# Optimization experiments

Hardware: AMD Instinct MI355X
Metric: run time of the kernel (lower is better)

The kernel has to match this reference:

```python
import jax, jax.numpy as jnp
import numpy as np

D_MODEL = 2048
NUM_HEADS = 32
NUM_KV_HEADS = 8
HEAD_DIM = D_MODEL // NUM_HEADS
ROPE_BASE = 10000.0


def _rope_cos_sin(T, dtype):
    # standard LLaMA-style RoPE tables, shape (1, 1, T, head_dim)
    half = HEAD_DIM // 2
    inv_freq = 1.0 / (ROPE_BASE ** (jnp.arange(0, half, dtype=jnp.float32) / half))
    pos = jnp.arange(T, dtype=jnp.float32)
    freqs = pos[:, None] * inv_freq[None, :]          # (T, half)
    emb = jnp.concatenate([freqs, freqs], axis=-1)     # (T, head_dim)
    cos = jnp.cos(emb)[None, None].astype(dtype)
    sin = jnp.sin(emb)[None, None].astype(dtype)
    return cos, sin


def _rotate_half(x):
    h = x.shape[-1] // 2
    return jnp.concatenate([-x[..., h:], x[..., :h]], axis=-1)


def setup_inputs() -> dict:
    key = jax.random.key(0)
    ks = jax.random.split(key, 5)
    B, T = 2, 2048
    s = 1.0 / np.sqrt(D_MODEL)
    return {
        "x": jax.random.normal(ks[0], (B, T, D_MODEL), jnp.float32),
        "Wq": jax.random.normal(ks[1], (D_MODEL, D_MODEL), jnp.float32) * s,
        "Wk": jax.random.normal(ks[2], (NUM_KV_HEADS * HEAD_DIM, D_MODEL), jnp.float32) * s,
        "Wv": jax.random.normal(ks[3], (NUM_KV_HEADS * HEAD_DIM, D_MODEL), jnp.float32) * s,
        "Wo": jax.random.normal(ks[4], (D_MODEL, D_MODEL), jnp.float32) * s,
    }


def reference(x, Wq, Wk, Wv, Wo):
    B, T, _ = x.shape
    # projections (torch Linear: y = x @ W.T)
    Q = (x @ Wq.T).reshape(B, T, NUM_HEADS, HEAD_DIM).transpose(0, 2, 1, 3)      # (B,H,T,D)
    K = (x @ Wk.T).reshape(B, T, NUM_KV_HEADS, HEAD_DIM).transpose(0, 2, 1, 3)   # (B,Hkv,T,D)
    V = (x @ Wv.T).reshape(B, T, NUM_KV_HEADS, HEAD_DIM).transpose(0, 2, 1, 3)

    cos, sin = _rope_cos_sin(T, x.dtype)
    Q = Q * cos + _rotate_half(Q) * sin
    K = K * cos + _rotate_half(K) * sin

    # GQA: expand kv heads to query heads
    heads_per_kv = NUM_HEADS // NUM_KV_HEADS
    group_map = jnp.arange(NUM_HEADS) // heads_per_kv
    K_sel = K[:, group_map]  # (B,H,T,D)
    V_sel = V[:, group_map]

    scale = 1.0 / np.sqrt(HEAD_DIM)
    scores = jnp.einsum("bhqd,bhkd->bhqk", Q, K_sel) * scale
    causal = jnp.tril(jnp.ones((T, T), dtype=bool))
    scores = jnp.where(causal, scores, jnp.finfo(scores.dtype).min)
    attn = jax.nn.softmax(scores, axis=-1)
    out = jnp.einsum("bhqk,bhkd->bhqd", attn, V_sel)
    out = out.transpose(0, 2, 1, 3).reshape(B, T, D_MODEL)
    return out @ Wo.T
```

## Files before the change

kernel.cpp:

```cpp
#include <hip/hip_runtime.h>
#include <stdint.h>


typedef unsigned short u16;
typedef __attribute__((ext_vector_type(8))) short short8;
typedef __attribute__((ext_vector_type(4))) float floatx4;

#define T_SEQ 2048
#define DMODEL 2048
#define NHEADS 32
#define KVHEADS 8
#define HDIM 64

__device__ __forceinline__ u16 f2bf(float f) {
  uint32_t u = __builtin_bit_cast(uint32_t, f);
  u = (u + 0x7FFFu + ((u >> 16) & 1u)) >> 16;
  return (u16)u;
}
__device__ __forceinline__ float bf2f(u16 h) {
  uint32_t u = ((uint32_t)h) << 16;
  return __builtin_bit_cast(float, u);
}

__device__ __forceinline__ void gld_lds16(const void* g, void* l) {
  __builtin_amdgcn_global_load_lds(
      (const __attribute__((address_space(1))) unsigned int*)g,
      (__attribute__((address_space(3))) unsigned int*)l, 16, 0, 0);
}

__global__ __launch_bounds__(256) void cvt_kernel(const float* __restrict__ src,
                                                  u16* __restrict__ dst, int n4) {
  int i = blockIdx.x * 256 + threadIdx.x;
  if (i >= n4) return;
  float4 v = ((const float4*)src)[i];
  ushort4 o;
  o.x = f2bf(v.x); o.y = f2bf(v.y); o.z = f2bf(v.z); o.w = f2bf(v.w);
  ((ushort4*)dst)[i] = o;
}

__global__ __launch_bounds__(256) void rope_table_kernel(float* __restrict__ cosT,
                                                         float* __restrict__ sinT) {
  int idx = blockIdx.x * 256 + threadIdx.x;
  int t = idx >> 5, i = idx & 31;
  float invf = 1.0f / powf(10000.0f, (float)i / 32.0f);
  float a = (float)t * invf;
  cosT[idx] = cosf(a);
  sinT[idx] = sinf(a);
}

template <bool OUT_F32>
__global__ __launch_bounds__(256) void gemm_bt(const u16* __restrict__ A,
                                               const u16* __restrict__ Bm,
                                               float* __restrict__ Cf,
                                               u16* __restrict__ Cb,
                                               int M, int N, int K) {
  __shared__ u16 As[128 * 64];
  __shared__ u16 Bs[128 * 64];
  const int tid = threadIdx.x;
  const int lane = tid & 63;
  const int wid = tid >> 6;
  const int wr = wid >> 1, wc = wid & 1;
  const long bm = (long)blockIdx.y * 128;
  const long bn = (long)blockIdx.x * 128;

  floatx4 acc[4][4] = {};

  for (int kt = 0; kt < K; kt += 64) {
#pragma unroll
    for (int c = 0; c < 4; ++c) {
      int g = (wid * 4 + c) * 64 + lane;
      int row = g >> 3, slot = g & 7;
      int ss = slot ^ (row & 7);
      gld_lds16(A + (bm + row) * (long)K + kt + ss * 8, (char*)As + g * 16);
      gld_lds16(Bm + (bn + row) * (long)K + kt + ss * 8, (char*)Bs + g * 16);
    }
    __syncthreads();
#pragma unroll
    for (int ks = 0; ks < 2; ++ks) {
      short8 af[4], bfr[4];
#pragma unroll
      for (int m = 0; m < 4; ++m) {
        int row = wr * 64 + m * 16 + (lane & 15);
        int slot = (ks * 4 + (lane >> 4)) ^ (row & 7);
        af[m] = *(const short8*)((const char*)As + row * 128 + slot * 16);
      }
#pragma unroll
      for (int n = 0; n < 4; ++n) {
        int row = wc * 64 + n * 16 + (lane & 15);
        int slot = (ks * 4 + (lane >> 4)) ^ (row & 7);
        bfr[n] = *(const short8*)((const char*)Bs + row * 128 + slot * 16);
      }
#pragma unroll
      for (int m = 0; m < 4; ++m)
#pragma unroll
        for (int n = 0; n < 4; ++n)
          acc[m][n] = __builtin_amdgcn_mfma_f32_16x16x32_bf16(af[m], bfr[n],
                                                              acc[m][n], 0, 0, 0);
    }
    __syncthreads();
  }
#pragma unroll
  for (int m = 0; m < 4; ++m)
#pragma unroll
    for (int n = 0; n < 4; ++n)
#pragma unroll
      for (int r = 0; r < 4; ++r) {
        long row = bm + wr * 64 + m * 16 + (lane >> 4) * 4 + r;
        long col = bn + wc * 64 + n * 16 + (lane & 15);
        if constexpr (OUT_F32)
          Cf[row * N + col] = acc[m][n][r];
        else
          Cb[row * N + col] = f2bf(acc[m][n][r]);
      }
}

__global__ __launch_bounds__(256) void rope_apply_kernel(
    const u16* __restrict__ QKV, const float* __restrict__ cosT,
    const float* __restrict__ sinT, u16* __restrict__ Qh, u16* __restrict__ Kh) {
  int idx = blockIdx.x * 256 + threadIdx.x;
  int c = idx % 2560;
  int bt = idx / 2560;
  int t = bt & (T_SEQ - 1);
  int b = bt >> 11;
  int hd = c & 63;
  int i = hd & 31;
  float cs = cosT[t * 32 + i];
  float sn = sinT[t * 32 + i];
  long base = (long)bt * 3072;
  float xv = bf2f(QKV[base + c]);
  int pairc = (hd < 32) ? c + 32 : c - 32;
  float xp = bf2f(QKV[base + pairc]);
  float rot = (hd < 32) ? -xp : xp;
  float ov = xv * cs + rot * sn;
  if (c < 2048) {
    int h = c >> 6;
    Qh[((long)(b * NHEADS + h) * T_SEQ + t) * HDIM + hd] = f2bf(ov);
  } else {
    int kv = (c - 2048) >> 6;
    Kh[((long)(b * KVHEADS + kv) * T_SEQ + t) * HDIM + hd] = f2bf(ov);
  }
}

__global__ __launch_bounds__(256) void v_transpose_kernel(const u16* __restrict__ QKV,
                                                          u16* __restrict__ Vt) {
  __shared__ u16 tl[64 * 65];
  int blk = blockIdx.x;
  int ttile = blk & 31;
  int kvh = (blk >> 5) & 7;
  int b = blk >> 8;
  int tid = threadIdx.x;
  long bt0 = (long)b * T_SEQ + ttile * 64;
#pragma unroll
  for (int j = 0; j < 2; ++j) {
    int chunk = tid * 2 + j;
    int el = chunk * 8;
    int row = el >> 6, col = el & 63;
    short8 v = *(const short8*)(QKV + (bt0 + row) * 3072 + 2560 + kvh * 64 + col);
#pragma unroll
    for (int k = 0; k < 8; ++k) tl[(col + k) * 65 + row] = (u16)v[k];
  }
  __syncthreads();
#pragma unroll
  for (int j = 0; j < 2; ++j) {
    int chunk = tid * 2 + j;
    int el = chunk * 8;
    int d = el >> 6, t0 = el & 63;
    short8 o;
#pragma unroll
    for (int k = 0; k < 8; ++k) o[k] = (short)tl[d * 65 + t0 + k];
    *(short8*)(Vt + ((long)(b * KVHEADS + kvh) * HDIM + d) * T_SEQ + ttile * 64 + t0) = o;
  }
}

__global__ __launch_bounds__(256) void attn_kernel(const u16* __restrict__ Qh,
                                                   const u16* __restrict__ Kh,
                                                   const u16* __restrict__ Vt,
                                                   u16* __restrict__ O) {
  __shared__ u16 Ks[64 * 64];
  __shared__ u16 Vs[64 * 64];
  __shared__ u16 Ps[4 * 1024];
  const int tid = threadIdx.x;
  const int lane = tid & 63;
  const int w = tid >> 6;
  const int blk = blockIdx.x;
  const int qb = blk & 31;
  const int h = (blk >> 5) & 31;
  const int b = blk >> 10;
  const int kvh = h >> 2;
  const int qbase = qb * 64;
  const int l15 = lane & 15;
  const int l4 = lane >> 4;

  const u16* Qp = Qh + ((long)(b * NHEADS + h) * T_SEQ + qbase + w * 16 + l15) * HDIM;
  short8 qf0 = *(const short8*)(Qp + l4 * 8);
  short8 qf1 = *(const short8*)(Qp + 32 + l4 * 8);
  const u16* Kbase = Kh + (long)(b * KVHEADS + kvh) * T_SEQ * HDIM;
  const u16* Vbase = Vt + (long)(b * KVHEADS + kvh) * HDIM * T_SEQ;

  float m_run = -1e30f, l_run = 0.f;
  floatx4 oA[4] = {};
  const int qg = qbase + w * 16 + l15;
  char* Pw = (char*)Ps + w * 2048;

  for (int kt = 0; kt <= qb; ++kt) {
#pragma unroll
    for (int c = 0; c < 2; ++c) {
      int g = (w * 2 + c) * 64 + lane;
      int row = g >> 3, slot = g & 7;
      int ss = slot ^ (row & 7);
      gld_lds16(Kbase + (long)(kt * 64 + row) * HDIM + ss * 8, (char*)Ks + g * 16);
      gld_lds16(Vbase + (long)row * T_SEQ + kt * 64 + ss * 8, (char*)Vs + g * 16);
    }
    __syncthreads();

    floatx4 st[4] = {};
#pragma unroll
    for (int ks = 0; ks < 2; ++ks) {
      short8 qf = ks ? qf1 : qf0;
#pragma unroll
      for (int tt = 0; tt < 4; ++tt) {
        int row = tt * 16 + l15;
        int slot = (ks * 4 + l4) ^ (row & 7);
        short8 kf = *(const short8*)((const char*)Ks + row * 128 + slot * 16);
        st[tt] = __builtin_amdgcn_mfma_f32_16x16x32_bf16(kf, qf, st[tt], 0, 0, 0);
      }
    }

    float p[4][4];
    float mt = -1e30f;
#pragma unroll
    for (int tt = 0; tt < 4; ++tt)
#pragma unroll
      for (int r = 0; r < 4; ++r) {
        int tg = kt * 64 + tt * 16 + l4 * 4 + r;
        float v = st[tt][r] * 0.125f;
        v = (tg <= qg) ? v : -1e30f;
        p[tt][r] = v;
        mt = fmaxf(mt, v);
      }
    mt = fmaxf(mt, __shfl_xor(mt, 16));
    mt = fmaxf(mt, __shfl_xor(mt, 32));
    float m_new = fmaxf(m_run, mt);
    float alpha = __expf(m_run - m_new);
    float lsum = 0.f;
#pragma unroll
    for (int tt = 0; tt < 4; ++tt)
#pragma unroll
      for (int r = 0; r < 4; ++r) {
        float e = __expf(p[tt][r] - m_new);
        p[tt][r] = e;
        lsum += e;
      }
    lsum += __shfl_xor(lsum, 16);
    lsum += __shfl_xor(lsum, 32);
    l_run = l_run * alpha + lsum;
    m_run = m_new;

#pragma unroll
    for (int tt = 0; tt < 4; ++tt) {
      uint2 pk;
      pk.x = (uint32_t)f2bf(p[tt][0]) | ((uint32_t)f2bf(p[tt][1]) << 16);
      pk.y = (uint32_t)f2bf(p[tt][2]) | ((uint32_t)f2bf(p[tt][3]) << 16);
      int t0 = tt * 16 + l4 * 4;
      int slot = (t0 >> 3) ^ (l15 & 7);
      int half = (t0 & 4) ? 8 : 0;
      *(uint2*)(Pw + l15 * 128 + slot * 16 + half) = pk;
    }
    asm volatile("s_waitcnt lgkmcnt(0)" ::: "memory");

    float a0 = __shfl(alpha, l4 * 4 + 0);
    float a1 = __shfl(alpha, l4 * 4 + 1);
    float a2 = __shfl(alpha, l4 * 4 + 2);
    float a3 = __shfl(alpha, l4 * 4 + 3);
#pragma unroll
    for (int dd = 0; dd < 4; ++dd) {
      oA[dd][0] *= a0; oA[dd][1] *= a1; oA[dd][2] *= a2; oA[dd][3] *= a3;
    }
#pragma unroll
    for (int ks2 = 0; ks2 < 2; ++ks2) {
      int slotp = (ks2 * 4 + l4) ^ (l15 & 7);
      short8 pa = *(const short8*)(Pw + l15 * 128 + slotp * 16);
#pragma unroll
      for (int dd = 0; dd < 4; ++dd) {
        int row = dd * 16 + l15;
        int slot = (ks2 * 4 + l4) ^ (row & 7);
        short8 vb = *(const short8*)((const char*)Vs + row * 128 + slot * 16);
        oA[dd] = __builtin_amdgcn_mfma_f32_16x16x32_bf16(pa, vb, oA[dd], 0, 0, 0);
      }
    }
    __syncthreads();
  }

  float linv = 1.0f / l_run;
  float i0 = __shfl(linv, l4 * 4 + 0);
  float i1 = __shfl(linv, l4 * 4 + 1);
  float i2 = __shfl(linv, l4 * 4 + 2);
  float i3 = __shfl(linv, l4 * 4 + 3);
  float iv[4] = {i0, i1, i2, i3};
#pragma unroll
  for (int dd = 0; dd < 4; ++dd)
#pragma unroll
    for (int r = 0; r < 4; ++r) {
      int trow = qbase + w * 16 + l4 * 4 + r;
      int col = h * 64 + dd * 16 + l15;
      O[((long)b * T_SEQ + trow) * DMODEL + col] = f2bf(oA[dd][r] * iv[r]);
    }
}

extern "C" void kernel_launch(void* const* d_in, const int* in_sizes, int n_in,
                              void* d_out, int out_size, void* d_ws, size_t ws_size,
                              hipStream_t stream) {
  const float* x = (const float*)d_in[0];
  const float* Wq = (const float*)d_in[1];
  const float* Wk = (const float*)d_in[2];
  const float* Wv = (const float*)d_in[3];
  const float* Wo = (const float*)d_in[4];
  float* out = (float*)d_out;

  char* ws = (char*)d_ws;
  u16* x_bf = (u16*)(ws);
  u16* Obuf = (u16*)(ws);
  u16* Wqkv_bf = (u16*)(ws + 16777216);
  u16* Wo_bf = (u16*)(ws + 29360128);
  u16* QKV = (u16*)(ws + 37748736);
  u16* Qh = (u16*)(ws + 62914560);
  u16* Kh = (u16*)(ws + 79691776);
  u16* Vt = (u16*)(ws + 83886080);
  float* cosT = (float*)(ws + 88080384);
  float* sinT = (float*)(ws + 88342528);

  cvt_kernel<<<8192, 256, 0, stream>>>(x, x_bf, 2097152);
  cvt_kernel<<<4096, 256, 0, stream>>>(Wq, Wqkv_bf, 1048576);
  cvt_kernel<<<1024, 256, 0, stream>>>(Wk, Wqkv_bf + 2048 * 2048, 262144);
  cvt_kernel<<<1024, 256, 0, stream>>>(Wv, Wqkv_bf + 2560 * 2048, 262144);
  cvt_kernel<<<4096, 256, 0, stream>>>(Wo, Wo_bf, 1048576);
  rope_table_kernel<<<256, 256, 0, stream>>>(cosT, sinT);

  dim3 g1(24, 32);
  gemm_bt<false><<<g1, 256, 0, stream>>>(x_bf, Wqkv_bf, nullptr, QKV, 4096, 3072, 2048);

  rope_apply_kernel<<<40960, 256, 0, stream>>>(QKV, cosT, sinT, Qh, Kh);
  v_transpose_kernel<<<512, 256, 0, stream>>>(QKV, Vt);

  attn_kernel<<<2048, 256, 0, stream>>>(Qh, Kh, Vt, Obuf);

  dim3 g2(16, 32);
  gemm_bt<true><<<g2, 256, 0, stream>>>(Obuf, Wo_bf, out, nullptr, 4096, 2048, 2048);
}
```

Measured before the change: 392.5 us.

## Double-buffer K/V tiles, reverse block order, and defer softmax rescaling

The attention kernel now double-buffers K/V tiles in LDS, prefetching the next tile while computing the current one. A single barrier per iteration replaces the previous sync-after-load pattern. Blocks are issued heaviest-first (reversed q-block order) to balance the causal workload. The causal mask is applied only on the diagonal tile, and the online-softmax rescale is skipped when the running max grows by no more than a threshold. MFMA sections also get s_setprio. The extra buffers double K/V LDS use, which may reduce occupancy, and deferred rescaling relies on bounded exponent growth for accuracy.

```diff
diff --git a/kernel.cpp b/kernel.cpp
--- a/kernel.cpp
+++ b/kernel.cpp
@@ -176,14 +176,14 @@
                                                    const u16* __restrict__ Kh,
                                                    const u16* __restrict__ Vt,
                                                    u16* __restrict__ O) {
-  __shared__ u16 Ks[64 * 64];
-  __shared__ u16 Vs[64 * 64];
+  __shared__ u16 Ks[2][64 * 64];
+  __shared__ u16 Vs[2][64 * 64];
   __shared__ u16 Ps[4 * 1024];
   const int tid = threadIdx.x;
   const int lane = tid & 63;
   const int w = tid >> 6;
   const int blk = blockIdx.x;
-  const int qb = blk & 31;
+  const int qb = 31 - (blk & 31);
   const int h = (blk >> 5) & 31;
   const int b = blk >> 10;
   const int kvh = h >> 2;
@@ -202,18 +202,33 @@
   const int qg = qbase + w * 16 + l15;
   char* Pw = (char*)Ps + w * 2048;
 
-  for (int kt = 0; kt <= qb; ++kt) {
+  auto STAGE = [&](int kt, int buf) {
 #pragma unroll
     for (int c = 0; c < 2; ++c) {
       int g = (w * 2 + c) * 64 + lane;
       int row = g >> 3, slot = g & 7;
       int ss = slot ^ (row & 7);
-      gld_lds16(Kbase + (long)(kt * 64 + row) * HDIM + ss * 8, (char*)Ks + g * 16);
-      gld_lds16(Vbase + (long)row * T_SEQ + kt * 64 + ss * 8, (char*)Vs + g * 16);
-    }
-    __syncthreads();
+      gld_lds16(Kbase + (long)(kt * 64 + row) * HDIM + ss * 8,
+                (char*)Ks[buf] + g * 16);
+      gld_lds16(Vbase + (long)row * T_SEQ + kt * 64 + ss * 8,
+                (char*)Vs[buf] + g * 16);
+    }
+  };
+
+  STAGE(0, 0);
+  asm volatile("s_waitcnt vmcnt(0)" ::: "memory");
+  __builtin_amdgcn_s_barrier();
+  asm volatile("" ::: "memory");
+
+  for (int kt = 0; kt <= qb; ++kt) {
+    const int cur = kt & 1;
+    if (kt < qb) STAGE(kt + 1, cur ^ 1);
+
+    const char* Kc = (const char*)Ks[cur];
+    const char* Vc = (const char*)Vs[cur];
 
     floatx4 st[4] = {};
+    __builtin_amdgcn_s_setprio(1);
 #pragma unroll
     for (int ks = 0; ks < 2; ++ks) {
       short8 qf = ks ? qf1 : qf0;
@@ -221,40 +236,60 @@
       for (int tt = 0; tt < 4; ++tt) {
         int row = tt * 16 + l15;
         int slot = (ks * 4 + l4) ^ (row & 7);
-        short8 kf = *(const short8*)((const char*)Ks + row * 128 + slot * 16);
+        short8 kf = *(const short8*)(Kc + row * 128 + slot * 16);
         st[tt] = __builtin_amdgcn_mfma_f32_16x16x32_bf16(kf, qf, st[tt], 0, 0, 0);
       }
     }
+    __builtin_amdgcn_s_setprio(0);
 
     float p[4][4];
     float mt = -1e30f;
-#pragma unroll
-    for (int tt = 0; tt < 4; ++tt)
-#pragma unroll
-      for (int r = 0; r < 4; ++r) {
-        int tg = kt * 64 + tt * 16 + l4 * 4 + r;
-        float v = st[tt][r] * 0.125f;
-        v = (tg <= qg) ? v : -1e30f;
-        p[tt][r] = v;
-        mt = fmaxf(mt, v);
-      }
+    if (kt == qb) {
+#pragma unroll
+      for (int tt = 0; tt < 4; ++tt)
+#pragma unroll
+        for (int r = 0; r < 4; ++r) {
+          int tg = kt * 64 + tt * 16 + l4 * 4 + r;
+          float v = st[tt][r] * 0.125f;
+          v = (tg <= qg) ? v : -1e30f;
+          p[tt][r] = v;
+          mt = fmaxf(mt, v);
+        }
+    } else {
+#pragma unroll
+      for (int tt = 0; tt < 4; ++tt)
+#pragma unroll
+        for (int r = 0; r < 4; ++r) {
+          float v = st[tt][r] * 0.125f;
+          p[tt][r] = v;
+          mt = fmaxf(mt, v);
+        }
+    }
     mt = fmaxf(mt, __shfl_xor(mt, 16));
     mt = fmaxf(mt, __shfl_xor(mt, 32));
-    float m_new = fmaxf(m_run, mt);
-    float alpha = __expf(m_run - m_new);
+
+    bool defer = __all(mt - m_run <= 8.0f);
+    float m_use, alpha;
+    if (defer) {
+      m_use = m_run;
+      alpha = 1.0f;
+    } else {
+      m_use = fmaxf(m_run, mt);
+      alpha = __expf(m_run - m_use);
+    }
     float lsum = 0.f;
 #pragma unroll
     for (int tt = 0; tt < 4; ++tt)
 #pragma unroll
       for (int r = 0; r < 4; ++r) {
-        float e = __expf(p[tt][r] - m_new);
+        float e = __expf(p[tt][r] - m_use);
         p[tt][r] = e;
         lsum += e;
       }
     lsum += __shfl_xor(lsum, 16);
     lsum += __shfl_xor(lsum, 32);
     l_run = l_run * alpha + lsum;
-    m_run = m_new;
+    m_run = m_use;
 
 #pragma unroll
     for (int tt = 0; tt < 4; ++tt) {
@@ -268,14 +303,17 @@
     }
     asm volatile("s_waitcnt lgkmcnt(0)" ::: "memory");
 
-    float a0 = __shfl(alpha, l4 * 4 + 0);
-    float a1 = __shfl(alpha, l4 * 4 + 1);
-    float a2 = __shfl(alpha, l4 * 4 + 2);
-    float a3 = __shfl(alpha, l4 * 4 + 3);
-#pragma unroll
-    for (int dd = 0; dd < 4; ++dd) {
-      oA[dd][0] *= a0; oA[dd][1] *= a1; oA[dd][2] *= a2; oA[dd][3] *= a3;
-    }
+    if (!defer) {
+      float a0 = __shfl(alpha, l4 * 4 + 0);
+      float a1 = __shfl(alpha, l4 * 4 + 1);
+      float a2 = __shfl(alpha, l4 * 4 + 2);
+      float a3 = __shfl(alpha, l4 * 4 + 3);
+#pragma unroll
+      for (int dd = 0; dd < 4; ++dd) {
+        oA[dd][0] *= a0; oA[dd][1] *= a1; oA[dd][2] *= a2; oA[dd][3] *= a3;
+      }
+    }
+    __builtin_amdgcn_s_setprio(1);
 #pragma unroll
     for (int ks2 = 0; ks2 < 2; ++ks2) {
       int slotp = (ks2 * 4 + l4) ^ (l15 & 7);
@@ -284,11 +322,15 @@
       for (int dd = 0; dd < 4; ++dd) {
         int row = dd * 16 + l15;
         int slot = (ks2 * 4 + l4) ^ (row & 7);
-        short8 vb = *(const short8*)((const char*)Vs + row * 128 + slot * 16);
+        short8 vb = *(const short8*)(Vc + row * 128 + slot * 16);
         oA[dd] = __builtin_amdgcn_mfma_f32_16x16x32_bf16(pa, vb, oA[dd], 0, 0, 0);
       }
     }
-    __syncthreads();
+    __builtin_amdgcn_s_setprio(0);
+
+    asm volatile("s_waitcnt vmcnt(0)" ::: "memory");
+    __builtin_amdgcn_s_barrier();
+    asm volatile("" ::: "memory");
   }
 
   float linv = 1.0f / l_run;
```

Result: faster. 376.8 us (-4.0%).

## Restructure attention loop: direct global K/V loads, exp2 softmax, lazy rescale, swizzle

Applied to the files above, without the earlier changes.

Folds the softmax scale and log2(e) into Q during the RoPE step so the attention loop can use exp2 directly. The attention kernel drops the shared-memory K/V staging and the block-wide barriers, and each wave now reads K and V fragments straight from global memory through the cache. It adds a deferred-max rescale that skips the alpha multiply when the running max grows by at most 8, applies the causal mask only on the diagonal tile, and adds MFMA priority hints. Blocks are reordered so the longest query tiles run first and neighbouring blocks share KV heads. The trade-off is redundant global/L2 traffic across the four waves in place of one shared LDS copy, and looser numeric bounds on the unnormalised exponentials.

```diff
diff --git a/kernel.cpp b/kernel.cpp
--- a/kernel.cpp
+++ b/kernel.cpp
@@ -11,6 +11,7 @@
 #define NHEADS 32
 #define KVHEADS 8
 #define HDIM 64
+#define QK_SCALE 0.1803368801111204f
 
 __device__ __forceinline__ u16 f2bf(float f) {
   uint32_t u = __builtin_bit_cast(uint32_t, f);
@@ -134,7 +135,7 @@
   float ov = xv * cs + rot * sn;
   if (c < 2048) {
     int h = c >> 6;
-    Qh[((long)(b * NHEADS + h) * T_SEQ + t) * HDIM + hd] = f2bf(ov);
+    Qh[((long)(b * NHEADS + h) * T_SEQ + t) * HDIM + hd] = f2bf(ov * QK_SCALE);
   } else {
     int kv = (c - 2048) >> 6;
     Kh[((long)(b * KVHEADS + kv) * T_SEQ + t) * HDIM + hd] = f2bf(ov);
@@ -172,20 +173,19 @@
   }
 }
 
-__global__ __launch_bounds__(256) void attn_kernel(const u16* __restrict__ Qh,
-                                                   const u16* __restrict__ Kh,
-                                                   const u16* __restrict__ Vt,
-                                                   u16* __restrict__ O) {
-  __shared__ u16 Ks[64 * 64];
-  __shared__ u16 Vs[64 * 64];
+__global__ __launch_bounds__(256, 4) void attn_kernel(const u16* __restrict__ Qh,
+                                                      const u16* __restrict__ Kh,
+                                                      const u16* __restrict__ Vt,
+                                                      u16* __restrict__ O) {
   __shared__ u16 Ps[4 * 1024];
   const int tid = threadIdx.x;
   const int lane = tid & 63;
   const int w = tid >> 6;
-  const int blk = blockIdx.x;
-  const int qb = blk & 31;
-  const int h = (blk >> 5) & 31;
-  const int b = blk >> 10;
+  const int blk0 = blockIdx.x;
+  const int swz = (blk0 & 7) * 256 + (blk0 >> 3);
+  const int qb = 31 - (swz & 31);
+  const int h = (swz >> 5) & 31;
+  const int b = swz >> 10;
   const int kvh = h >> 2;
   const int qbase = qb * 64;
   const int l15 = lane & 15;
@@ -203,64 +203,64 @@
   char* Pw = (char*)Ps + w * 2048;
 
   for (int kt = 0; kt <= qb; ++kt) {
-#pragma unroll
-    for (int c = 0; c < 2; ++c) {
-      int g = (w * 2 + c) * 64 + lane;
-      int row = g >> 3, slot = g & 7;
-      int ss = slot ^ (row & 7);
-      gld_lds16(Kbase + (long)(kt * 64 + row) * HDIM + ss * 8, (char*)Ks + g * 16);
-      gld_lds16(Vbase + (long)row * T_SEQ + kt * 64 + ss * 8, (char*)Vs + g * 16);
-    }
-    __syncthreads();
+    const u16* Kt = Kbase + (long)kt * 64 * HDIM;
+    const u16* Vti = Vbase + kt * 64;
 
     floatx4 st[4] = {};
+    __builtin_amdgcn_s_setprio(1);
 #pragma unroll
     for (int ks = 0; ks < 2; ++ks) {
       short8 qf = ks ? qf1 : qf0;
 #pragma unroll
       for (int tt = 0; tt < 4; ++tt) {
-        int row = tt * 16 + l15;
-        int slot = (ks * 4 + l4) ^ (row & 7);
-        short8 kf = *(const short8*)((const char*)Ks + row * 128 + slot * 16);
+        short8 kf = *(const short8*)(Kt + (tt * 16 + l15) * HDIM + ks * 32 + l4 * 8);
         st[tt] = __builtin_amdgcn_mfma_f32_16x16x32_bf16(kf, qf, st[tt], 0, 0, 0);
       }
     }
-
-    float p[4][4];
-    float mt = -1e30f;
-#pragma unroll
-    for (int tt = 0; tt < 4; ++tt)
-#pragma unroll
-      for (int r = 0; r < 4; ++r) {
-        int tg = kt * 64 + tt * 16 + l4 * 4 + r;
-        float v = st[tt][r] * 0.125f;
-        v = (tg <= qg) ? v : -1e30f;
-        p[tt][r] = v;
-        mt = fmaxf(mt, v);
-      }
+    __builtin_amdgcn_s_setprio(0);
+
+    if (kt == qb) {
+#pragma unroll
+      for (int tt = 0; tt < 4; ++tt)
+#pragma unroll
+        for (int r = 0; r < 4; ++r) {
+          int tg = kt * 64 + tt * 16 + l4 * 4 + r;
+          if (tg > qg) st[tt][r] = -1e30f;
+        }
+    }
+    float mx0 = fmaxf(fmaxf(st[0][0], st[0][1]), fmaxf(st[0][2], st[0][3]));
+    float mx1 = fmaxf(fmaxf(st[1][0], st[1][1]), fmaxf(st[1][2], st[1][3]));
+    float mx2 = fmaxf(fmaxf(st[2][0], st[2][1]), fmaxf(st[2][2], st[2][3]));
+    float mx3 = fmaxf(fmaxf(st[3][0], st[3][1]), fmaxf(st[3][2], st[3][3]));
+    float mt = fmaxf(fmaxf(mx0, mx1), fmaxf(mx2, mx3));
     mt = fmaxf(mt, __shfl_xor(mt, 16));
     mt = fmaxf(mt, __shfl_xor(mt, 32));
-    float m_new = fmaxf(m_run, mt);
-    float alpha = __expf(m_run - m_new);
-    float lsum = 0.f;
-#pragma unroll
-    for (int tt = 0; tt < 4; ++tt)
-#pragma unroll
-      for (int r = 0; r < 4; ++r) {
-        float e = __expf(p[tt][r] - m_new);
-        p[tt][r] = e;
-        lsum += e;
-      }
+
+    bool defer = __all(mt - m_run <= 8.0f);
+    float m_use = defer ? m_run : fmaxf(m_run, mt);
+    float alpha = defer ? 1.0f : exp2f(m_run - m_use);
+
+    float lsp[4];
+#pragma unroll
+    for (int tt = 0; tt < 4; ++tt) {
+      float e0 = exp2f(st[tt][0] - m_use);
+      float e1 = exp2f(st[tt][1] - m_use);
+      float e2 = exp2f(st[tt][2] - m_use);
+      float e3 = exp2f(st[tt][3] - m_use);
+      st[tt][0] = e0; st[tt][1] = e1; st[tt][2] = e2; st[tt][3] = e3;
+      lsp[tt] = (e0 + e1) + (e2 + e3);
+    }
+    float lsum = (lsp[0] + lsp[1]) + (lsp[2] + lsp[3]);
     lsum += __shfl_xor(lsum, 16);
     lsum += __shfl_xor(lsum, 32);
     l_run = l_run * alpha + lsum;
-    m_run = m_new;
+    m_run = m_use;
 
 #pragma unroll
     for (int tt = 0; tt < 4; ++tt) {
       uint2 pk;
-      pk.x = (uint32_t)f2bf(p[tt][0]) | ((uint32_t)f2bf(p[tt][1]) << 16);
-      pk.y = (uint32_t)f2bf(p[tt][2]) | ((uint32_t)f2bf(p[tt][3]) << 16);
+      pk.x = (uint32_t)f2bf(st[tt][0]) | ((uint32_t)f2bf(st[tt][1]) << 16);
+      pk.y = (uint32_t)f2bf(st[tt][2]) | ((uint32_t)f2bf(st[tt][3]) << 16);
       int t0 = tt * 16 + l4 * 4;
       int slot = (t0 >> 3) ^ (l15 & 7);
       int half = (t0 & 4) ? 8 : 0;
@@ -268,27 +268,29 @@
     }
     asm volatile("s_waitcnt lgkmcnt(0)" ::: "memory");
 
-    float a0 = __shfl(alpha, l4 * 4 + 0);
-    float a1 = __shfl(alpha, l4 * 4 + 1);
-    float a2 = __shfl(alpha, l4 * 4 + 2);
-    float a3 = __shfl(alpha, l4 * 4 + 3);
-#pragma unroll
-    for (int dd = 0; dd < 4; ++dd) {
-      oA[dd][0] *= a0; oA[dd][1] *= a1; oA[dd][2] *= a2; oA[dd][3] *= a3;
-    }
+    if (!defer) {
+      float a0 = __shfl(alpha, l4 * 4 + 0);
+      float a1 = __shfl(alpha, l4 * 4 + 1);
+      float a2 = __shfl(alpha, l4 * 4 + 2);
+      float a3 = __shfl(alpha, l4 * 4 + 3);
+#pragma unroll
+      for (int dd = 0; dd < 4; ++dd) {
+        oA[dd][0] *= a0; oA[dd][1] *= a1; oA[dd][2] *= a2; oA[dd][3] *= a3;
+      }
+    }
+
+    __builtin_amdgcn_s_setprio(1);
 #pragma unroll
     for (int ks2 = 0; ks2 < 2; ++ks2) {
       int slotp = (ks2 * 4 + l4) ^ (l15 & 7);
       short8 pa = *(const short8*)(Pw + l15 * 128 + slotp * 16);
 #pragma unroll
       for (int dd = 0; dd < 4; ++dd) {
-        int row = dd * 16 + l15;
-        int slot = (ks2 * 4 + l4) ^ (row & 7);
-        short8 vb = *(const short8*)((const char*)Vs + row * 128 + slot * 16);
+        short8 vb = *(const short8*)(Vti + (dd * 16 + l15) * (long)T_SEQ + ks2 * 32 + l4 * 8);
         oA[dd] = __builtin_amdgcn_mfma_f32_16x16x32_bf16(pa, vb, oA[dd], 0, 0, 0);
       }
     }
-    __syncthreads();
+    __builtin_amdgcn_s_setprio(0);
   }
 
   float linv = 1.0f / l_run;
```

Measured after the change: 569.6 us. 45.1% more time.
